# Optimization experiments

Hardware: AMD Instinct MI355X
Metric: run time of the kernel (lower is better)

Reference implementation:

```python
import jax, jax.numpy as jnp
import numpy as np

SHIFT, REDUCE = 3, 2
B, L, E, H = 64, 512, 300, 256


def _make_transitions():
    # Left-branching valid parse: S S R S R S R ... (L shifts, L-1 reduces)
    T = 2 * L - 1
    tr = np.full(T, REDUCE, dtype=np.int64)
    tr[0] = SHIFT
    tr[1::2] = SHIFT
    return jnp.asarray(np.tile(tr[None, :], (B, 1)))


def setup_inputs() -> dict:
    key = jax.random.key(0)
    ks = jax.random.split(key, 5)
    s = 0.05
    return {
        "sentence": jax.random.normal(ks[0], (B, L, E), jnp.float32),
        "transitions": _make_transitions(),
        "W_word": jax.random.normal(ks[1], (E, 2 * H), jnp.float32) * s,
        "b_word": jnp.zeros((2 * H,), jnp.float32),
        "W_left": jax.random.normal(ks[2], (H, 5 * H), jnp.float32) * s,
        "W_right": jax.random.normal(ks[3], (H, 5 * H), jnp.float32) * s,
        "b_reduce": jnp.zeros((5 * H,), jnp.float32),
    }


def reference(sentence, transitions, W_word, b_word, W_left, W_right, b_reduce):
    Bsz, Ls, _ = sentence.shape
    Hs = W_left.shape[0]
    proj = sentence @ W_word + b_word                  # [B, L, 2H] (word projection; BN/dropout disabled)
    h_buf, c_buf = jnp.split(proj, 2, axis=2)          # buffers, each [B, L, H]
    T = transitions.shape[1]
    bidx = jnp.arange(Bsz)

    def step(carry, trans_t):
        sh, sc, ptr, bp = carry                        # thin stacks [B,T+2,H], pointers [B]
        shift = trans_t == SHIFT
        i1 = jnp.maximum(ptr - 1, 0)                   # right child (stack top)
        i2 = jnp.maximum(ptr - 2, 0)                   # left child
        hl, cl = sh[bidx, i2], sc[bidx, i2]
        hr, cr = sh[bidx, i1], sc[bidx, i1]
        g = hl @ W_left + hr @ W_right + b_reduce      # [B, 5H] TreeLSTM gates
        ig, flg, frg, og, ug = jnp.split(g, 5, axis=1)
        c_red = (jax.nn.sigmoid(flg) * cl + jax.nn.sigmoid(frg) * cr
                 + jax.nn.sigmoid(ig) * jnp.tanh(ug))
        h_red = jax.nn.sigmoid(og) * jnp.tanh(c_red)
        bsafe = jnp.minimum(bp, Ls - 1)
        val_h = jnp.where(shift[:, None], h_buf[bidx, bsafe], h_red)
        val_c = jnp.where(shift[:, None], c_buf[bidx, bsafe], c_red)
        pos = jnp.where(shift, ptr, i2)                # shift pushes at ptr; reduce writes at ptr-2
        sh = sh.at[bidx, pos].set(val_h)
        sc = sc.at[bidx, pos].set(val_c)
        ptr = ptr + jnp.where(shift, 1, -1)
        bp = bp + shift.astype(bp.dtype)
        return (sh, sc, ptr, bp), None

    sh0 = jnp.zeros((Bsz, T + 2, Hs), sentence.dtype)
    sc0 = jnp.zeros((Bsz, T + 2, Hs), sentence.dtype)
    ptr0 = jnp.zeros((Bsz,), jnp.int32)
    bp0 = jnp.zeros((Bsz,), jnp.int32)
    (sh, sc, ptr, _), _ = jax.lax.scan(
        step, (sh0, sc0, ptr0, bp0), jnp.swapaxes(transitions, 0, 1))
    return sh[bidx, jnp.maximum(ptr - 1, 0)]           # final stack top h: [B, H]
```

## Files before the change

### kernel.cpp

```cpp
#include <hip/hip_runtime.h>
#include <hip/hip_bf16.h>
#include <math.h>

#define BSZ   64
#define LSEQ  512
#define EDIM  300
#define HDIM  256
#define TLEN  1023
#define PROJW 512
#define GW    1280

#define NROW  8
#define NHID  8
#define NRG   8
#define NBLK  256
#define SLOTS 2

#define PROJ_N   (BSZ*LSEQ*PROJW)
#define STACKF   PROJ_N
#define PAIRB    (STACKF/2)
#define PAIR_CNT (2*BSZ*SLOTS*HDIM)

#define NODEBIT 0x80000000u
#define SENT    0xFFFFFFFFu
#define LROW    264
#define HRO     (NROW*LROW + 4)
#define RPITCH  328
#define RROW    41

__global__ void __launch_bounds__(256)
proj_gemm(const float* __restrict__ A, const float* __restrict__ W,
          const float* __restrict__ bias, float* __restrict__ out) {
    __shared__ float As[8][65];
    __shared__ float Bs[8][64];
    const int tid = threadIdx.x;
    const int tx = tid & 15, ty = tid >> 4;
    const int bm = blockIdx.y, bn = blockIdx.x;

    float acc[4][4] = {};
    const int e  = tid * 2;
    const int ar = e >> 3, ac = e & 7;
    const int br = e >> 6, bc = e & 63;

    for (int k0 = 0; k0 < EDIM; k0 += 8) {
        __syncthreads();
        {
            const float* Ap = A + (size_t)(bm * 64 + ar) * EDIM;
            int gk = k0 + ac;
            As[ac][ar]     = (gk     < EDIM) ? Ap[gk]     : 0.f;
            As[ac + 1][ar] = (gk + 1 < EDIM) ? Ap[gk + 1] : 0.f;
            int gkb = k0 + br;
            float w0 = 0.f, w1 = 0.f;
            if (gkb < EDIM) {
                const float* Wp = W + (size_t)gkb * PROJW + bn * 64;
                w0 = Wp[bc]; w1 = Wp[bc + 1];
            }
            Bs[br][bc] = w0; Bs[br][bc + 1] = w1;
        }
        __syncthreads();
        #pragma unroll
        for (int kk = 0; kk < 8; ++kk) {
            float a[4], b[4];
            #pragma unroll
            for (int i = 0; i < 4; ++i) a[i] = As[kk][ty * 4 + i];
            #pragma unroll
            for (int j = 0; j < 4; ++j) b[j] = Bs[kk][tx * 4 + j];
            #pragma unroll
            for (int i = 0; i < 4; ++i)
                #pragma unroll
                for (int j = 0; j < 4; ++j)
                    acc[i][j] += a[i] * b[j];
        }
    }
    #pragma unroll
    for (int i = 0; i < 4; ++i) {
        const int row  = bm * 64 + ty * 4 + i;
        const int col0 = bn * 64 + tx * 4;
        float* op = out + (size_t)row * PROJW + col0;
        #pragma unroll
        for (int j = 0; j < 4; ++j) op[j] = acc[i][j] + bias[col0 + j];
    }
}

__device__ __forceinline__ int qswz(int Q, int row) {
    return Q ^ row ^ ((Q >> 3) & 7);
}

__device__ __forceinline__ unsigned long long pld(const unsigned long long* p) {
    return __hip_atomic_load(p, __ATOMIC_RELAXED, __HIP_MEMORY_SCOPE_AGENT);
}

__device__ __forceinline__ void fetch_octet(const unsigned long long* pb,
                                            unsigned ee, float* h) {
    while ((unsigned)(pld(pb) >> 32) < ee)
        __builtin_amdgcn_s_sleep(1);
    for (;;) {
        unsigned long long v[8];
        #pragma unroll
        for (int i = 0; i < 8; ++i) v[i] = pld(pb + i);
        bool ok = true;
        #pragma unroll
        for (int i = 0; i < 8; ++i) ok &= ((unsigned)(v[i] >> 32) >= ee);
        if (ok) {
            #pragma unroll
            for (int i = 0; i < 8; ++i) h[i] = __uint_as_float((unsigned)v[i]);
            return;
        }
        __builtin_amdgcn_s_sleep(1);
    }
}

__global__ void __launch_bounds__(256, 1)
scan_coop(const int* __restrict__ trans,
          const float* __restrict__ Wl, const float* __restrict__ Wr,
          const float* __restrict__ bred,
          float* __restrict__ ws, float* __restrict__ out) {
    __shared__ __align__(16) float hbuf[HRO + NROW * LROW];
    __shared__ __align__(16) float red[16 * RPITCH];
    __shared__ float    cstk[2 * SLOTS * NROW * NHID];
    __shared__ unsigned tbits[NROW][32];
    __shared__ unsigned fbits[32];
    __shared__ short    tg[NROW][SLOTS];
    __shared__ unsigned eps[NROW][SLOTS];
    __shared__ unsigned d_hl[NROW], d_hr[NROW], d_wr[NROW];
    __shared__ unsigned e_hl[NROW], e_hr[NROW];
    __shared__ unsigned c_l[NROW], c_r[NROW], cw[NROW];
    __shared__ unsigned d_oh[NROW], e_oh[NROW];
    __shared__ int      isred[NROW];

    const int tid   = threadIdx.x;
    const int rg    = blockIdx.x & 7;
    const int cs    = blockIdx.x >> 3;
    const int rbase = rg * NROW;
    const int n0    = cs * NHID;

    const int srow = tid >> 5, sc = tid & 31;
    const int colq = tid & 7;
    const int rh   = (tid >> 3) & 1;
    const int m    = (tid >> 4) & 1;
    const int w8   = tid >> 5;
    const int gn   = n0 + colq;
    const int orow = tid >> 3;

    unsigned long long* p64 = (unsigned long long*)ws;

    float4 w[8][5];
    {
        const float* src = (m == 0) ? Wl : Wr;
        const int kbase = w8 * 32;
        #pragma unroll
        for (int j = 0; j < 8; ++j) {
            const int k0 = kbase + j * 4;
            #pragma unroll
            for (int g = 0; g < 5; ++g) {
                w[j][g].x = src[(size_t)(k0 + 0) * GW + g * HDIM + gn];
                w[j][g].y = src[(size_t)(k0 + 1) * GW + g * HDIM + gn];
                w[j][g].z = src[(size_t)(k0 + 2) * GW + g * HDIM + gn];
                w[j][g].w = src[(size_t)(k0 + 3) * GW + g * HDIM + gn];
            }
        }
    }
    #pragma unroll
    for (int j = 0; j < 8; ++j)
        #pragma unroll
        for (int g = 0; g < 5; ++g)
            asm volatile("" : "+v"(w[j][g].x), "+v"(w[j][g].y),
                              "+v"(w[j][g].z), "+v"(w[j][g].w));

    if (tid < NROW * 32) {
        const int r2 = tid >> 5, wd = tid & 31;
        unsigned bits = 0;
        for (int j = 0; j < 32; ++j) {
            const int t = wd * 32 + j;
            if (t < TLEN && trans[(size_t)(rbase + r2) * TLEN + t] == 3) bits |= (1u << j);
        }
        tbits[r2][wd] = bits;
    }
    if (tid < NROW) {
        tg[tid][0] = -3; tg[tid][1] = -3;
        eps[tid][0] = 0; eps[tid][1] = 0;
        isred[tid] = 0;
    }
    __syncthreads();
    if (tid < 32) {
        unsigned fb = 0;
        #pragma unroll
        for (int r2 = 0; r2 < NROW; ++r2) fb |= ~tbits[r2][tid];
        if (tid == 31) fb &= 0x7FFFFFFFu;
        fbits[tid] = fb;
    }

    float bv[5];
    #pragma unroll
    for (int g = 0; g < 5; ++g) bv[g] = bred[g * HDIM + gn];

    int ptr = 0, bp = 0;
    unsigned nbar = 0;
    __syncthreads();

    for (int t = 0; t < TLEN; ++t) {
        const int redstep = (fbits[t >> 5] >> (t & 31)) & 1;
        if (redstep) ++nbar;

        if (tid < NROW) {
            const int r = tid, grow = rbase + r;
            const int is_shift = (tbits[r][t >> 5] >> (t & 31)) & 1;
            if (is_shift) {
                int pos = ptr; if (pos < 0) pos = 0; if (pos > SLOTS - 1) pos = SLOTS - 1;
                tg[r][pos] = (short)min(bp, LSEQ - 1);
                ptr++; bp++;
                isred[r] = 0;
            } else {
                const int i1 = min(max(ptr - 1, 0), SLOTS - 1);
                const int i2 = min(max(ptr - 2, 0), SLOTS - 1);
                const short t1 = tg[r][i1], t2 = tg[r][i2];
                unsigned dl, el = 0, cdl;
                if (t2 >= 0)       { dl = (unsigned)((grow * LSEQ + (int)t2) * PROJW); cdl = dl + HDIM; }
                else if (t2 <= -3) { dl = SENT; cdl = SENT; }
                else { const int par = (t2 == -2);
                       dl = NODEBIT | (unsigned)(PAIRB + ((par * BSZ + grow) * SLOTS + i2) * HDIM);
                       el = eps[r][i2];
                       cdl = NODEBIT | (unsigned)(par * 2 + i2); }
                unsigned dr, er = 0, cdr;
                if (t1 >= 0)       { dr = (unsigned)((grow * LSEQ + (int)t1) * PROJW); cdr = dr + HDIM; }
                else if (t1 <= -3) { dr = SENT; cdr = SENT; }
                else { const int par = (t1 == -2);
                       dr = NODEBIT | (unsigned)(PAIRB + ((par * BSZ + grow) * SLOTS + i1) * HDIM);
                       er = eps[r][i1];
                       cdr = NODEBIT | (unsigned)(par * 2 + i1); }
                d_hl[r] = dl; e_hl[r] = el; c_l[r] = cdl;
                d_hr[r] = dr; e_hr[r] = er; c_r[r] = cdr;
                const int pnew = (t2 == -1) ? 1 : 0;
                d_wr[r] = (unsigned)(PAIRB + ((pnew * BSZ + grow) * SLOTS + i2) * HDIM);
                cw[r]   = (unsigned)(pnew * 2 + i2);
                eps[r][i2] = nbar;
                tg[r][i2] = (short)(pnew ? -2 : -1);
                ptr--;
                isred[r] = 1;
            }
        }
        __syncthreads();

        if (!redstep) continue;

        float clw = 0.f, crw = 0.f;
        if (tid < 64 && isred[orow]) {
            const unsigned cdl = c_l[orow], cdr = c_r[orow];
            if (cdl != SENT && !(cdl & NODEBIT)) clw = ws[cdl + gn];
            if (cdr != SENT && !(cdr & NODEBIT)) crw = ws[cdr + gn];
        }

        if (isred[srow]) {
            const unsigned oh0 = d_hl[srow], oh1 = d_hr[srow];
            const bool nd0 = (oh0 != SENT) && (oh0 & NODEBIT);
            const bool nd1 = (oh1 != SENT) && (oh1 & NODEBIT);
            float h0[8], h1[8];

            if (oh0 == SENT) {
                #pragma unroll
                for (int i = 0; i < 8; ++i) h0[i] = 0.f;
            } else if (!nd0) {
                const float4 a = *(const float4*)(ws + oh0 + sc * 8);
                const float4 b = *(const float4*)(ws + oh0 + sc * 8 + 4);
                h0[0]=a.x; h0[1]=a.y; h0[2]=a.z; h0[3]=a.w;
                h0[4]=b.x; h0[5]=b.y; h0[6]=b.z; h0[7]=b.w;
            }
            if (oh1 == SENT) {
                #pragma unroll
                for (int i = 0; i < 8; ++i) h1[i] = 0.f;
            } else if (!nd1) {
                const float4 a = *(const float4*)(ws + oh1 + sc * 8);
                const float4 b = *(const float4*)(ws + oh1 + sc * 8 + 4);
                h1[0]=a.x; h1[1]=a.y; h1[2]=a.z; h1[3]=a.w;
                h1[4]=b.x; h1[5]=b.y; h1[6]=b.z; h1[7]=b.w;
            }
            if (nd0) fetch_octet(p64 + (oh0 & ~NODEBIT) + sc * 8, e_hl[srow], h0);
            if (nd1) fetch_octet(p64 + (oh1 & ~NODEBIT) + sc * 8, e_hr[srow], h1);

            *(float4*)&hbuf[srow * LROW + 4 * qswz(2 * sc + 0, srow)] =
                make_float4(h0[0], h0[1], h0[2], h0[3]);
            *(float4*)&hbuf[srow * LROW + 4 * qswz(2 * sc + 1, srow)] =
                make_float4(h0[4], h0[5], h0[6], h0[7]);
            *(float4*)&hbuf[HRO + srow * LROW + 4 * qswz(2 * sc + 0, srow)] =
                make_float4(h1[0], h1[1], h1[2], h1[3]);
            *(float4*)&hbuf[HRO + srow * LROW + 4 * qswz(2 * sc + 1, srow)] =
                make_float4(h1[4], h1[5], h1[6], h1[7]);
        }
        __syncthreads();

        float acc[4][5];
        #pragma unroll
        for (int r = 0; r < 4; ++r)
            #pragma unroll
            for (int g = 0; g < 5; ++g) acc[r][g] = 0.f;
        {
            const float* hb = hbuf + m * HRO;
            #pragma unroll
            for (int j = 0; j < 8; ++j) {
                const int kq = w8 * 8 + j;
                #pragma unroll
                for (int r = 0; r < 4; ++r) {
                    const int row = rh * 4 + r;
                    const float4 x = *(const float4*)&hb[row * LROW + 4 * qswz(kq, row)];
                    #pragma unroll
                    for (int g = 0; g < 5; ++g)
                        acc[r][g] += x.x * w[j][g].x + x.y * w[j][g].y
                                   + x.z * w[j][g].z + x.w * w[j][g].w;
                }
            }
        }
        {
            const int g16 = w8 * 2 + m;
            #pragma unroll
            for (int r = 0; r < 4; ++r) {
                const int row = rh * 4 + r;
                #pragma unroll
                for (int g = 0; g < 5; ++g)
                    red[g16 * RPITCH + row * RROW + colq * 5 + g] = acc[r][g];
            }
        }
        __syncthreads();

        if (tid < 64) {
            if (isred[orow]) {
                float s[5];
                #pragma unroll
                for (int g = 0; g < 5; ++g) s[g] = bv[g];
                #pragma unroll
                for (int q = 0; q < 16; ++q)
                    #pragma unroll
                    for (int g = 0; g < 5; ++g)
                        s[g] += red[q * RPITCH + orow * RROW + colq * 5 + g];
                const unsigned cdl = c_l[orow], cdr = c_r[orow];
                const float cl = (cdl == SENT) ? 0.f :
                    ((cdl & NODEBIT) ? cstk[((cdl & 3) * NROW + orow) * NHID + colq] : clw);
                const float cr = (cdr == SENT) ? 0.f :
                    ((cdr & NODEBIT) ? cstk[((cdr & 3) * NROW + orow) * NHID + colq] : crw);
                const float si = 1.f / (1.f + expf(-s[0]));
                const float sl = 1.f / (1.f + expf(-s[1]));
                const float sr = 1.f / (1.f + expf(-s[2]));
                const float so = 1.f / (1.f + expf(-s[3]));
                const float c_red = sl * cl + sr * cr + si * tanhf(s[4]);
                const float h_red = so * tanhf(c_red);
                cstk[(cw[orow] * NROW + orow) * NHID + colq] = c_red;
                const unsigned long long pv =
                    ((unsigned long long)nbar << 32) | (unsigned long long)__float_as_uint(h_red);
                __hip_atomic_store(p64 + d_wr[orow] + gn, pv,
                                   __ATOMIC_RELAXED, __HIP_MEMORY_SCOPE_AGENT);
            }
        }
    }

    if (tid < NROW) {
        const int top = min(max(ptr - 1, 0), SLOTS - 1);
        const short tt = tg[tid][top];
        const int grow = rbase + tid;
        if (tt >= 0)       { d_oh[tid] = (unsigned)((grow * LSEQ + (int)tt) * PROJW); e_oh[tid] = 0; }
        else if (tt <= -3) { d_oh[tid] = SENT; e_oh[tid] = 0; }
        else { const int par = (tt == -2);
               d_oh[tid] = NODEBIT | (unsigned)(PAIRB + ((par * BSZ + grow) * SLOTS + top) * HDIM);
               e_oh[tid] = eps[tid][top]; }
    }
    __syncthreads();
    if (tid < 64) {
        const int ocol = n0 + (tid & 7);
        const unsigned oh = d_oh[orow];
        float v;
        if (oh == SENT) v = 0.f;
        else if (!(oh & NODEBIT)) v = ws[oh + ocol];
        else {
            const unsigned long long* pb = p64 + (oh & ~NODEBIT) + ocol;
            const unsigned ee = e_oh[orow];
            unsigned long long pv;
            for (;;) {
                pv = pld(pb);
                if ((unsigned)(pv >> 32) >= ee) break;
                __builtin_amdgcn_s_sleep(1);
            }
            v = __uint_as_float((unsigned)pv);
        }
        out[(size_t)(rbase + orow) * HDIM + ocol] = v;
    }
}

extern "C" void kernel_launch(void* const* d_in, const int* in_sizes, int n_in,
                              void* d_out, int out_size, void* d_ws, size_t ws_size,
                              hipStream_t stream) {
    const float* sentence    = (const float*)d_in[0];
    const int*   transitions = (const int*)  d_in[1];
    const float* W_word      = (const float*)d_in[2];
    const float* b_word      = (const float*)d_in[3];
    const float* W_left      = (const float*)d_in[4];
    const float* W_right     = (const float*)d_in[5];
    const float* b_reduce    = (const float*)d_in[6];
    float* out  = (float*)d_out;
    float* ws_f = (float*)d_ws;

    hipMemsetAsync((char*)d_ws + (size_t)STACKF * 4, 0,
                   (size_t)PAIR_CNT * 8, stream);

    dim3 g1(PROJW / 64, (BSZ * LSEQ) / 64);
    proj_gemm<<<g1, 256, 0, stream>>>(sentence, W_word, b_word, ws_f);

    scan_coop<<<NBLK, 256, 0, stream>>>(transitions, W_left, W_right, b_reduce,
                                        ws_f, out);
}
```

Before: 3.059 ms.

## Precompute reduce descriptors per epoch and prefetch next epoch's operands

The sequential per-step stack bookkeeping is moved into a prologue that builds per-epoch descriptor tables in shared memory, so the main loop iterates only over reduce epochs. The loop also stages the next epoch's child h values right after the current epoch's finalization, which removes one barrier per epoch and overlaps polling with the tail of the step. Finalization is spread across four waves (16 lanes each) instead of one. The trade-off is a larger shared-memory descriptor table capped at DMAX epochs, plus the risk of ordering bugs from staging before the other blocks' writes are visible.

```diff
diff --git a/kernel.cpp b/kernel.cpp
--- a/kernel.cpp
+++ b/kernel.cpp
@@ -12,17 +12,18 @@
 
 #define NROW  8
 #define NHID  8
-#define NRG   8
 #define NBLK  256
 #define SLOTS 2
+#define DMAX  512
 
 #define PROJ_N   (BSZ*LSEQ*PROJW)
 #define STACKF   PROJ_N
 #define PAIRB    (STACKF/2)
 #define PAIR_CNT (2*BSZ*SLOTS*HDIM)
 
+#define TSENT   0xFFFFu
+#define SENT    0xFFFFFFFFu
 #define NODEBIT 0x80000000u
-#define SENT    0xFFFFFFFFu
 #define LROW    264
 #define HRO     (NROW*LROW + 4)
 #define RPITCH  328
@@ -85,15 +86,11 @@
 __device__ __forceinline__ int qswz(int Q, int row) {
     return Q ^ row ^ ((Q >> 3) & 7);
 }
-
 __device__ __forceinline__ unsigned long long pld(const unsigned long long* p) {
     return __hip_atomic_load(p, __ATOMIC_RELAXED, __HIP_MEMORY_SCOPE_AGENT);
 }
-
 __device__ __forceinline__ void fetch_octet(const unsigned long long* pb,
                                             unsigned ee, float* h) {
-    while ((unsigned)(pld(pb) >> 32) < ee)
-        __builtin_amdgcn_s_sleep(1);
     for (;;) {
         unsigned long long v[8];
         #pragma unroll
@@ -117,16 +114,11 @@
           float* __restrict__ ws, float* __restrict__ out) {
     __shared__ __align__(16) float hbuf[HRO + NROW * LROW];
     __shared__ __align__(16) float red[16 * RPITCH];
-    __shared__ float    cstk[2 * SLOTS * NROW * NHID];
+    __shared__ float    cstk[4 * NROW * NHID];
     __shared__ unsigned tbits[NROW][32];
     __shared__ unsigned fbits[32];
-    __shared__ short    tg[NROW][SLOTS];
-    __shared__ unsigned eps[NROW][SLOTS];
-    __shared__ unsigned d_hl[NROW], d_hr[NROW], d_wr[NROW];
-    __shared__ unsigned e_hl[NROW], e_hr[NROW];
-    __shared__ unsigned c_l[NROW], c_r[NROW], cw[NROW];
+    __shared__ unsigned desc[DMAX][NROW][3];
     __shared__ unsigned d_oh[NROW], e_oh[NROW];
-    __shared__ int      isred[NROW];
 
     const int tid   = threadIdx.x;
     const int rg    = blockIdx.x & 7;
@@ -140,7 +132,12 @@
     const int m    = (tid >> 4) & 1;
     const int w8   = tid >> 5;
     const int gn   = n0 + colq;
-    const int orow = tid >> 3;
+    const int wv   = tid >> 6;
+    const int lane = tid & 63;
+    const bool fin = (lane < 16);
+    const int frow = 2 * wv + (lane >> 3);
+    const int fcol = lane & 7;
+    const int fgn  = n0 + fcol;
 
     unsigned long long* p64 = (unsigned long long*)ws;
 
@@ -176,11 +173,6 @@
         }
         tbits[r2][wd] = bits;
     }
-    if (tid < NROW) {
-        tg[tid][0] = -3; tg[tid][1] = -3;
-        eps[tid][0] = 0; eps[tid][1] = 0;
-        isred[tid] = 0;
-    }
     __syncthreads();
     if (tid < 32) {
         unsigned fb = 0;
@@ -189,104 +181,135 @@
         if (tid == 31) fb &= 0x7FFFFFFFu;
         fbits[tid] = fb;
     }
+    __syncthreads();
+    unsigned EPOCHS = 0;
+    for (int i = 0; i < 32; ++i) EPOCHS += (unsigned)__popc(fbits[i]);
+    if (EPOCHS > DMAX - 1) EPOCHS = DMAX - 1;
+
+    if (tid < NROW) {
+        const int r = tid, grow = rbase + r;
+        int ptr = 0, bp = 0;
+        unsigned tg0 = TSENT, tg1 = TSENT;
+        unsigned ep0 = 0, ep1 = 0;
+        unsigned n = 0;
+        for (int t = 0; t < TLEN; ++t) {
+            const int redstep = (fbits[t >> 5] >> (t & 31)) & 1;
+            if (redstep) ++n;
+            const int is_shift = (tbits[r][t >> 5] >> (t & 31)) & 1;
+            if (is_shift) {
+                const int pos = max(0, min(ptr, SLOTS - 1));
+                const unsigned wt = (unsigned)min(bp, LSEQ - 1);
+                if (pos == 0) tg0 = wt; else tg1 = wt;
+                ptr++; bp++;
+                if (redstep && n < DMAX) desc[n][r][2] = 0;
+            } else {
+                const int i1 = min(max(ptr - 1, 0), SLOTS - 1);
+                const int i2 = min(max(ptr - 2, 0), SLOTS - 1);
+                const unsigned t1 = i1 ? tg1 : tg0;
+                const unsigned t2 = i2 ? tg1 : tg0;
+                const unsigned e1 = i1 ? ep1 : ep0;
+                const unsigned e2 = i2 ? ep1 : ep0;
+                const int t2node = (t2 != TSENT) && (t2 & 0x8000u);
+                const int pnew = (t2node && !((t2 >> 1) & 1)) ? 1 : 0;
+                if (n < DMAX) {
+                    desc[n][r][0] = t2 | (t1 << 16);
+                    desc[n][r][1] = e2 | (e1 << 16);
+                    desc[n][r][2] = 1u | ((unsigned)(pnew * 2 + i2) << 1);
+                }
+                const unsigned newtag = 0x8000u | ((unsigned)pnew << 1) | (unsigned)i2;
+                if (i2 == 0) { tg0 = newtag; ep0 = n; }
+                else         { tg1 = newtag; ep1 = n; }
+                ptr--;
+            }
+        }
+        const int top = min(max(ptr - 1, 0), SLOTS - 1);
+        const unsigned tt = top ? tg1 : tg0;
+        const unsigned te = top ? ep1 : ep0;
+        if (tt == TSENT) { d_oh[r] = SENT; e_oh[r] = 0; }
+        else if (!(tt & 0x8000u)) {
+            d_oh[r] = (unsigned)((grow * LSEQ + (int)tt) * PROJW); e_oh[r] = 0;
+        } else {
+            d_oh[r] = NODEBIT | (unsigned)(PAIRB +
+                      ((((tt >> 1) & 1) * BSZ + grow) * SLOTS + (tt & 1)) * HDIM);
+            e_oh[r] = te;
+        }
+    }
+    __syncthreads();
 
     float bv[5];
     #pragma unroll
     for (int g = 0; g < 5; ++g) bv[g] = bred[g * HDIM + gn];
 
-    int ptr = 0, bp = 0;
-    unsigned nbar = 0;
-    __syncthreads();
-
-    for (int t = 0; t < TLEN; ++t) {
-        const int redstep = (fbits[t >> 5] >> (t & 31)) & 1;
-        if (redstep) ++nbar;
-
-        if (tid < NROW) {
-            const int r = tid, grow = rbase + r;
-            const int is_shift = (tbits[r][t >> 5] >> (t & 31)) & 1;
-            if (is_shift) {
-                int pos = ptr; if (pos < 0) pos = 0; if (pos > SLOTS - 1) pos = SLOTS - 1;
-                tg[r][pos] = (short)min(bp, LSEQ - 1);
-                ptr++; bp++;
-                isred[r] = 0;
-            } else {
-                const int i1 = min(max(ptr - 1, 0), SLOTS - 1);
-                const int i2 = min(max(ptr - 2, 0), SLOTS - 1);
-                const short t1 = tg[r][i1], t2 = tg[r][i2];
-                unsigned dl, el = 0, cdl;
-                if (t2 >= 0)       { dl = (unsigned)((grow * LSEQ + (int)t2) * PROJW); cdl = dl + HDIM; }
-                else if (t2 <= -3) { dl = SENT; cdl = SENT; }
-                else { const int par = (t2 == -2);
-                       dl = NODEBIT | (unsigned)(PAIRB + ((par * BSZ + grow) * SLOTS + i2) * HDIM);
-                       el = eps[r][i2];
-                       cdl = NODEBIT | (unsigned)(par * 2 + i2); }
-                unsigned dr, er = 0, cdr;
-                if (t1 >= 0)       { dr = (unsigned)((grow * LSEQ + (int)t1) * PROJW); cdr = dr + HDIM; }
-                else if (t1 <= -3) { dr = SENT; cdr = SENT; }
-                else { const int par = (t1 == -2);
-                       dr = NODEBIT | (unsigned)(PAIRB + ((par * BSZ + grow) * SLOTS + i1) * HDIM);
-                       er = eps[r][i1];
-                       cdr = NODEBIT | (unsigned)(par * 2 + i1); }
-                d_hl[r] = dl; e_hl[r] = el; c_l[r] = cdl;
-                d_hr[r] = dr; e_hr[r] = er; c_r[r] = cdr;
-                const int pnew = (t2 == -1) ? 1 : 0;
-                d_wr[r] = (unsigned)(PAIRB + ((pnew * BSZ + grow) * SLOTS + i2) * HDIM);
-                cw[r]   = (unsigned)(pnew * 2 + i2);
-                eps[r][i2] = nbar;
-                tg[r][i2] = (short)(pnew ? -2 : -1);
-                ptr--;
-                isred[r] = 1;
-            }
-        }
+    auto stage = [&](unsigned e) {
+        const unsigned dsc2 = desc[e][srow][2];
+        if (!(dsc2 & 1)) return;
+        const unsigned dsc0 = desc[e][srow][0];
+        const unsigned dsc1 = desc[e][srow][1];
+        const unsigned tagL = dsc0 & 0xFFFFu, tagR = dsc0 >> 16;
+        const unsigned eeL = dsc1 & 0xFFFFu, eeR = dsc1 >> 16;
+        const int grow = rbase + srow;
+        const bool ndL = (tagL != TSENT) && (tagL & 0x8000u);
+        const bool ndR = (tagR != TSENT) && (tagR & 0x8000u);
+        float h0[8], h1[8];
+
+        if (tagL == TSENT) {
+            #pragma unroll
+            for (int i = 0; i < 8; ++i) h0[i] = 0.f;
+        } else if (!ndL) {
+            const float* p = ws + (size_t)(grow * LSEQ + (int)tagL) * PROJW + sc * 8;
+            const float4 a = *(const float4*)p;
+            const float4 b = *(const float4*)(p + 4);
+            h0[0]=a.x; h0[1]=a.y; h0[2]=a.z; h0[3]=a.w;
+            h0[4]=b.x; h0[5]=b.y; h0[6]=b.z; h0[7]=b.w;
+        }
+        if (tagR == TSENT) {
+            #pragma unroll
+            for (int i = 0; i < 8; ++i) h1[i] = 0.f;
+        } else if (!ndR) {
+            const float* p = ws + (size_t)(grow * LSEQ + (int)tagR) * PROJW + sc * 8;
+            const float4 a = *(const float4*)p;
+            const float4 b = *(const float4*)(p + 4);
+            h1[0]=a.x; h1[1]=a.y; h1[2]=a.z; h1[3]=a.w;
+            h1[4]=b.x; h1[5]=b.y; h1[6]=b.z; h1[7]=b.w;
+        }
+        if (ndL)
+            fetch_octet(p64 + PAIRB +
+                ((((tagL >> 1) & 1) * BSZ + grow) * SLOTS + (tagL & 1)) * HDIM + sc * 8,
+                eeL, h0);
+        if (ndR)
+            fetch_octet(p64 + PAIRB +
+                ((((tagR >> 1) & 1) * BSZ + grow) * SLOTS + (tagR & 1)) * HDIM + sc * 8,
+                eeR, h1);
+
+        *(float4*)&hbuf[srow * LROW + 4 * qswz(2 * sc + 0, srow)] =
+            make_float4(h0[0], h0[1], h0[2], h0[3]);
+        *(float4*)&hbuf[srow * LROW + 4 * qswz(2 * sc + 1, srow)] =
+            make_float4(h0[4], h0[5], h0[6], h0[7]);
+        *(float4*)&hbuf[HRO + srow * LROW + 4 * qswz(2 * sc + 0, srow)] =
+            make_float4(h1[0], h1[1], h1[2], h1[3]);
+        *(float4*)&hbuf[HRO + srow * LROW + 4 * qswz(2 * sc + 1, srow)] =
+            make_float4(h1[4], h1[5], h1[6], h1[7]);
+    };
+
+    if (EPOCHS >= 1) stage(1);
+
+    for (unsigned e = 1; e <= EPOCHS; ++e) {
         __syncthreads();
 
-        if (!redstep) continue;
-
         float clw = 0.f, crw = 0.f;
-        if (tid < 64 && isred[orow]) {
-            const unsigned cdl = c_l[orow], cdr = c_r[orow];
-            if (cdl != SENT && !(cdl & NODEBIT)) clw = ws[cdl + gn];
-            if (cdr != SENT && !(cdr & NODEBIT)) crw = ws[cdr + gn];
-        }
-
-        if (isred[srow]) {
-            const unsigned oh0 = d_hl[srow], oh1 = d_hr[srow];
-            const bool nd0 = (oh0 != SENT) && (oh0 & NODEBIT);
-            const bool nd1 = (oh1 != SENT) && (oh1 & NODEBIT);
-            float h0[8], h1[8];
-
-            if (oh0 == SENT) {
-                #pragma unroll
-                for (int i = 0; i < 8; ++i) h0[i] = 0.f;
-            } else if (!nd0) {
-                const float4 a = *(const float4*)(ws + oh0 + sc * 8);
-                const float4 b = *(const float4*)(ws + oh0 + sc * 8 + 4);
-                h0[0]=a.x; h0[1]=a.y; h0[2]=a.z; h0[3]=a.w;
-                h0[4]=b.x; h0[5]=b.y; h0[6]=b.z; h0[7]=b.w;
-            }
-            if (oh1 == SENT) {
-                #pragma unroll
-                for (int i = 0; i < 8; ++i) h1[i] = 0.f;
-            } else if (!nd1) {
-                const float4 a = *(const float4*)(ws + oh1 + sc * 8);
-                const float4 b = *(const float4*)(ws + oh1 + sc * 8 + 4);
-                h1[0]=a.x; h1[1]=a.y; h1[2]=a.z; h1[3]=a.w;
-                h1[4]=b.x; h1[5]=b.y; h1[6]=b.z; h1[7]=b.w;
-            }
-            if (nd0) fetch_octet(p64 + (oh0 & ~NODEBIT) + sc * 8, e_hl[srow], h0);
-            if (nd1) fetch_octet(p64 + (oh1 & ~NODEBIT) + sc * 8, e_hr[srow], h1);
-
-            *(float4*)&hbuf[srow * LROW + 4 * qswz(2 * sc + 0, srow)] =
-                make_float4(h0[0], h0[1], h0[2], h0[3]);
-            *(float4*)&hbuf[srow * LROW + 4 * qswz(2 * sc + 1, srow)] =
-                make_float4(h0[4], h0[5], h0[6], h0[7]);
-            *(float4*)&hbuf[HRO + srow * LROW + 4 * qswz(2 * sc + 0, srow)] =
-                make_float4(h1[0], h1[1], h1[2], h1[3]);
-            *(float4*)&hbuf[HRO + srow * LROW + 4 * qswz(2 * sc + 1, srow)] =
-                make_float4(h1[4], h1[5], h1[6], h1[7]);
-        }
-        __syncthreads();
+        unsigned fd2 = 0, ftagL = TSENT, ftagR = TSENT;
+        if (fin) {
+            fd2 = desc[e][frow][2];
+            if (fd2 & 1) {
+                const unsigned d0 = desc[e][frow][0];
+                ftagL = d0 & 0xFFFFu; ftagR = d0 >> 16;
+                const int fg = rbase + frow;
+                if (ftagL != TSENT && !(ftagL & 0x8000u))
+                    clw = ws[(size_t)(fg * LSEQ + (int)ftagL) * PROJW + HDIM + fgn];
+                if (ftagR != TSENT && !(ftagR & 0x8000u))
+                    crw = ws[(size_t)(fg * LSEQ + (int)ftagR) * PROJW + HDIM + fgn];
+            }
+        }
 
         float acc[4][5];
         #pragma unroll
@@ -321,48 +344,45 @@
         }
         __syncthreads();
 
-        if (tid < 64) {
-            if (isred[orow]) {
-                float s[5];
+        if (fin && (fd2 & 1)) {
+            float s[5];
+            #pragma unroll
+            for (int g = 0; g < 5; ++g) s[g] = bv[g];
+            #pragma unroll
+            for (int q = 0; q < 16; ++q)
                 #pragma unroll
-                for (int g = 0; g < 5; ++g) s[g] = bv[g];
-                #pragma unroll
-                for (int q = 0; q < 16; ++q)
-                    #pragma unroll
-                    for (int g = 0; g < 5; ++g)
-                        s[g] += red[q * RPITCH + orow * RROW + colq * 5 + g];
-                const unsigned cdl = c_l[orow], cdr = c_r[orow];
-                const float cl = (cdl == SENT) ? 0.f :
-                    ((cdl & NODEBIT) ? cstk[((cdl & 3) * NROW + orow) * NHID + colq] : clw);
-                const float cr = (cdr == SENT) ? 0.f :
-                    ((cdr & NODEBIT) ? cstk[((cdr & 3) * NROW + orow) * NHID + colq] : crw);
-                const float si = 1.f / (1.f + expf(-s[0]));
-                const float sl = 1.f / (1.f + expf(-s[1]));
-                const float sr = 1.f / (1.f + expf(-s[2]));
-                const float so = 1.f / (1.f + expf(-s[3]));
-                const float c_red = sl * cl + sr * cr + si * tanhf(s[4]);
-                const float h_red = so * tanhf(c_red);
-                cstk[(cw[orow] * NROW + orow) * NHID + colq] = c_red;
-                const unsigned long long pv =
-                    ((unsigned long long)nbar << 32) | (unsigned long long)__float_as_uint(h_red);
-                __hip_atomic_store(p64 + d_wr[orow] + gn, pv,
-                                   __ATOMIC_RELAXED, __HIP_MEMORY_SCOPE_AGENT);
-            }
-        }
-    }
-
-    if (tid < NROW) {
-        const int top = min(max(ptr - 1, 0), SLOTS - 1);
-        const short tt = tg[tid][top];
-        const int grow = rbase + tid;
-        if (tt >= 0)       { d_oh[tid] = (unsigned)((grow * LSEQ + (int)tt) * PROJW); e_oh[tid] = 0; }
-        else if (tt <= -3) { d_oh[tid] = SENT; e_oh[tid] = 0; }
-        else { const int par = (tt == -2);
-               d_oh[tid] = NODEBIT | (unsigned)(PAIRB + ((par * BSZ + grow) * SLOTS + top) * HDIM);
-               e_oh[tid] = eps[tid][top]; }
-    }
+                for (int g = 0; g < 5; ++g)
+                    s[g] += red[q * RPITCH + frow * RROW + fcol * 5 + g];
+            float cl;
+            if (ftagL == TSENT) cl = 0.f;
+            else if (ftagL & 0x8000u) cl = cstk[((ftagL & 3u) * NROW + frow) * NHID + fcol];
+            else cl = clw;
+            float cr;
+            if (ftagR == TSENT) cr = 0.f;
+            else if (ftagR & 0x8000u) cr = cstk[((ftagR & 3u) * NROW + frow) * NHID + fcol];
+            else cr = crw;
+            const float si = 1.f / (1.f + expf(-s[0]));
+            const float sl = 1.f / (1.f + expf(-s[1]));
+            const float sr = 1.f / (1.f + expf(-s[2]));
+            const float so = 1.f / (1.f + expf(-s[3]));
+            const float c_red = sl * cl + sr * cr + si * tanhf(s[4]);
+            const float h_red = so * tanhf(c_red);
+            const unsigned cw = (fd2 >> 1) & 3u;
+            cstk[(cw * NROW + frow) * NHID + fcol] = c_red;
+            const unsigned dwr = (unsigned)(PAIRB +
+                (((cw >> 1) * BSZ + (rbase + frow)) * SLOTS + (cw & 1)) * HDIM);
+            const unsigned long long pv =
+                ((unsigned long long)e << 32) | (unsigned long long)__float_as_uint(h_red);
+            __hip_atomic_store(p64 + dwr + fgn, pv,
+                               __ATOMIC_RELAXED, __HIP_MEMORY_SCOPE_AGENT);
+        }
+        if (e < EPOCHS) stage(e + 1);
+    }
+
     __syncthreads();
+
     if (tid < 64) {
+        const int orow = tid >> 3;
         const int ocol = n0 + (tid & 7);
         const unsigned oh = d_oh[orow];
         float v;
```

After: 2.900 ms. 5.2% less time.
